# Optimization experiments

Hardware: AMD Instinct MI355X
Metric: run time of the kernel (lower is better)

Reference implementation:

```python
import jax, jax.numpy as jnp
import numpy as np

H = 100      # STATE_SIZE
ATT = 100    # ATTENTION_SIZE
E = 32       # EMBEDDINGS_SIZE
V = 50257    # char vocab
TV = 60      # tag vocab
N = 2048     # source length (incl EOS padding)
T = 2048     # target length (incl EOS padding)
TT = 64      # number of tags


def lstm_cell(x, h, c, Wih, Whh, b):
    # torch gate order: i, f, g, o
    z = x @ Wih.T + h @ Whh.T + b
    i, f, g, o = jnp.split(z, 4)
    c = jax.nn.sigmoid(f) * c + jax.nn.sigmoid(i) * jnp.tanh(g)
    h = jax.nn.sigmoid(o) * jnp.tanh(c)
    return h, c


def lstm_scan(xs, Wih, Whh, b):
    Hs = Whh.shape[1]
    def step(carry, x):
        h, c = lstm_cell(x, carry[0], carry[1], Wih, Whh, b)
        return (h, c), h
    init = (jnp.zeros(Hs, xs.dtype), jnp.zeros(Hs, xs.dtype))
    _, ys = jax.lax.scan(step, init, xs)
    return ys


def setup_inputs() -> dict:
    key = jax.random.key(0)
    ks = iter(jax.random.split(key, 40))
    def rn(shape, s=0.1):
        return jax.random.normal(next(ks), shape, jnp.float32) * s
    return {
        "src_ids": jax.random.randint(next(ks), (1, N), 0, V),
        "tag_ids": jax.random.randint(next(ks), (1, TT), 0, TV),
        "out_ids": jax.random.randint(next(ks), (1, T), 0, V),
        "weight": jnp.ones((), jnp.float32),
        "emb_char": rn((V, E)),
        "emb_tag": rn((TV, E)),
        "enc_f_Wih": rn((4 * H, E)), "enc_f_Whh": rn((4 * H, H)), "enc_f_b": rn((4 * H,)),
        "enc_b_Wih": rn((4 * H, E)), "enc_b_Whh": rn((4 * H, H)), "enc_b_b": rn((4 * H,)),
        "tag_Wih": rn((4 * H, E)), "tag_Whh": rn((4 * H, H)), "tag_b": rn((4 * H,)),
        "dec_Wih": rn((4 * H, 3 * H + E)), "dec_Whh": rn((4 * H, H)), "dec_b": rn((4 * H,)),
        "attn_w1": rn((ATT, 2 * H)), "attn_w2": rn((ATT, 2 * H)), "attn_w3": rn((ATT, 5)),
        "attn_v": rn((1, ATT)),
        "tag_attn_w1": rn((ATT, H)), "tag_attn_w2": rn((ATT, 2 * H)), "tag_attn_v": rn((1, ATT)),
        "out_W": rn((V, H)), "out_b": rn((V,)),
    }


def reference(src_ids, tag_ids, out_ids, weight, emb_char, emb_tag,
              enc_f_Wih, enc_f_Whh, enc_f_b, enc_b_Wih, enc_b_Whh, enc_b_b,
              tag_Wih, tag_Whh, tag_b, dec_Wih, dec_Whh, dec_b,
              attn_w1, attn_w2, attn_w3, attn_v,
              tag_attn_w1, tag_attn_w2, tag_attn_v, out_W, out_b):
    x = emb_char[src_ids[0]]                       # (N, E)
    tg = emb_tag[tag_ids[0]]                       # (TT, E)
    # bidirectional char encoder
    yf = lstm_scan(x, enc_f_Wih, enc_f_Whh, enc_f_b)
    yb = lstm_scan(x[::-1], enc_b_Wih, enc_b_Whh, enc_b_b)[::-1]
    enc = jnp.concatenate([yf, yb], -1)            # (N, 2H)
    # tag encoder + self-attention residual (matches self_encode_tags)
    tv = lstm_scan(tg, tag_Wih, tag_Whh, tag_b)    # (TT, H)
    sa = jax.nn.softmax(tv @ tv.T, axis=-1)
    tagv = tv + jnp.einsum('sh,st->th', tv, sa)    # (TT, H)
    w1dt = enc @ attn_w1.T                         # (N, ATT)
    tag_w1dt = tagv @ tag_attn_w1.T                # (TT, ATT)
    eos_emb = emb_char[0]
    # initial decoder step on (enc_last, tag_last, eos_emb) with zero state
    x0 = jnp.concatenate([enc[-1], tagv[-1], eos_emb])
    h0, c0 = lstm_cell(x0, jnp.zeros(H, jnp.float32), jnp.zeros(H, jnp.float32),
                       dec_Wih, dec_Whh, dec_b)
    # teacher forcing: previous output embedding (EOS=id 0 at t=0)
    prev_ids = jnp.concatenate([jnp.zeros((1,), out_ids.dtype), out_ids[0, :-1]])
    prev_emb = emb_char[prev_ids]                  # (T, E)

    def step(carry, inp):
        h, c, prev_att = carry
        pe, oid = inp
        state = jnp.concatenate([h, c])            # (2H,)
        # tag attention
        taw = jax.nn.softmax(jnp.tanh(tag_w1dt + state @ tag_attn_w2.T) @ tag_attn_v[0])
        tag_ctx = taw @ tagv                       # (H,)
        new_state = state + jnp.concatenate([tag_ctx, tag_ctx])
        # char attention with 5-wide previous-attention feature
        scores = jnp.tanh(w1dt + new_state @ attn_w2.T + prev_att @ attn_w3.T) @ attn_v[0]
        aw = jax.nn.softmax(scores)                # (N,)
        ctx = aw @ enc                             # (2H,)
        startt = jnp.clip(jnp.argmax(aw) - 1, 0, N - 6)
        new_prev = jax.lax.dynamic_slice(aw, (startt,), (5,))
        hn, cn = lstm_cell(jnp.concatenate([ctx, tag_ctx, pe]), h, c,
                           dec_Wih, dec_Whh, dec_b)
        logits = hn @ out_W.T + out_b              # (V,)
        lt = -jax.nn.log_softmax(logits)[oid]
        return (hn, cn, new_prev), lt

    _, losses = jax.lax.scan(step, (h0, c0, jnp.zeros(5, jnp.float32)),
                             (prev_emb, out_ids[0]))
    return jnp.sum(losses) * weight
```

## Files before the change

### kernel.cpp

```cpp
#include <hip/hip_runtime.h>
#include <math.h>

#define NN   2048
#define TLEN 2048
#define TTAG 64
#define VOC  50257
#define GW   32
#define CHK  64
#define RECU 80
static_assert(GW * CHK == NN, "chunking");

#define OFF_XF    0
#define OFF_XB    (OFF_XF  + NN*400)
#define OFF_TGX   (OFF_XB  + NN*400)
#define OFF_PEW   (OFF_TGX + TTAG*400)
#define OFF_ENC   (OFF_PEW + TLEN*400)
#define OFF_W1DT  (OFF_ENC + NN*200)
#define OFF_TAGV  (OFF_W1DT+ NN*100)
#define OFF_TGW1  (OFF_TAGV+ TTAG*100)
#define OFF_TGW   (OFF_TGW1+ TTAG*100)
#define OFF_HOUT  (OFF_TGW + TTAG*400)
#define OFF_REC   (OFF_HOUT+ TLEN*100)
#define OFF_HC    (OFF_REC + 2*GW*RECU*2)
#define OFF_FLG   (OFF_HC  + 2*128*2)
#define OFF_PB    (OFF_FLG + 4096)


__device__ __forceinline__ float rcpf(float x){ return __builtin_amdgcn_rcpf(x); }
__device__ __forceinline__ float sigf(float x){ return rcpf(1.0f+__expf(-x)); }
__device__ __forceinline__ float tanhfast(float x){
  float e = __expf(2.0f*x);
  return 1.0f - 2.0f*rcpf(e+1.0f);
}
__device__ __forceinline__ unsigned short f2b(float x){
  unsigned b=__float_as_uint(x);
  return (unsigned short)((b + 0x7fffu + ((b>>16)&1u))>>16);
}
__device__ __forceinline__ unsigned pk2(float a,float b){ return (unsigned)f2b(a) | ((unsigned)f2b(b)<<16); }
__device__ __forceinline__ float blo(unsigned u){ return __uint_as_float(u<<16); }
__device__ __forceinline__ float bhi(unsigned u){ return __uint_as_float(u&0xffff0000u); }

__device__ __forceinline__ unsigned long long ald64(const unsigned long long* p){
  return __hip_atomic_load(p,__ATOMIC_RELAXED,__HIP_MEMORY_SCOPE_SYSTEM);
}
__device__ __forceinline__ void ast64(unsigned long long* p, unsigned long long v){
  __hip_atomic_store(p,v,__ATOMIC_RELAXED,__HIP_MEMORY_SCOPE_SYSTEM);
}
__device__ __forceinline__ void vm0(){ asm volatile("s_waitcnt vmcnt(0)" ::: "memory"); }

__global__ void kInit(float* ws){
  unsigned long long* f = (unsigned long long*)(ws + OFF_FLG);
  int i = blockIdx.x*256 + threadIdx.x;
  if (i < 2048) ast64(f+i, 0ull);
}

__global__ __launch_bounds__(512) void kPrep(
    const int* src, const int* tag, const int* oid,
    const float* emb_char, const float* emb_tag,
    const float* fWih, const float* fb,
    const float* bWih, const float* bb,
    const float* tWih, const float* tb,
    const float* dWih, const float* db, float* ws)
{
  int r = blockIdx.x, j = threadIdx.x;
  if (j >= 400) return;
  if (r < NN) {
    const float* e = emb_char + (size_t)src[r]*32;
    const float* Wr = fWih + j*32;
    float a = fb[j];
    #pragma unroll
    for (int q=0;q<32;q++) a += e[q]*Wr[q];
    ws[OFF_XF + r*400 + j] = a;
  } else if (r < 2*NN) {
    int n = r - NN;
    const float* e = emb_char + (size_t)src[n]*32;
    const float* Wr = bWih + j*32;
    float a = bb[j];
    #pragma unroll
    for (int q=0;q<32;q++) a += e[q]*Wr[q];
    ws[OFF_XB + n*400 + j] = a;
  } else if (r < 2*NN + TTAG) {
    int s = r - 2*NN;
    const float* e = emb_tag + (size_t)tag[s]*32;
    const float* Wr = tWih + j*32;
    float a = tb[j];
    #pragma unroll
    for (int q=0;q<32;q++) a += e[q]*Wr[q];
    ws[OFF_TGX + s*400 + j] = a;
  } else {
    int t = r - (2*NN + TTAG);
    int pid = (t==0) ? 0 : oid[t-1];
    const float* e = emb_char + (size_t)pid*32;
    const float* Wr = dWih + (size_t)j*332 + 300;
    float a = db[j];
    #pragma unroll
    for (int q=0;q<32;q++) a += e[q]*Wr[q];
    ws[OFF_PEW + t*400 + j] = a;
  }
}

struct EncShared {
  float tvs[TTAG*100];
  float sa [TTAG*64];
  float hbuf[100];
  float zbuf[400];
};

__device__ void lstm_block(const float* Whh, const float* xbase, float* ws,
                           int reverse, int col, EncShared* sh)
{
  int tid = threadIdx.x;
  float whh[100];
  if (tid < 400){
    #pragma unroll
    for (int k=0;k<100;k++) whh[k] = Whh[tid*100+k];
  }
  float c = 0.f;
  if (tid < 100) sh->hbuf[tid] = 0.f;
  __syncthreads();
  for (int i=0;i<NN;i++){
    int n = reverse ? (NN-1-i) : i;
    if (tid < 400){
      float z = xbase[n*400+tid];
      #pragma unroll
      for (int k=0;k<100;k++) z += whh[k]*sh->hbuf[k];
      sh->zbuf[tid] = z;
    }
    __syncthreads();
    if (tid < 100){
      float zi=sh->zbuf[tid], zf=sh->zbuf[tid+100], zg=sh->zbuf[tid+200], zo=sh->zbuf[tid+300];
      c = sigf(zf)*c + sigf(zi)*tanhfast(zg);
      float h = sigf(zo)*tanhfast(c);
      sh->hbuf[tid] = h;
      ws[OFF_ENC + n*200 + col + tid] = h;
    }
    __syncthreads();
  }
}

__global__ __launch_bounds__(512,1) void kEnc(
    const float* fWhh, const float* bWhh, const float* tWhh,
    const float* taw1, const float* dWih, float* ws)
{
  __shared__ EncShared sh;
  int b = blockIdx.x, tid = threadIdx.x;
  if (b == 0){ lstm_block(fWhh, ws+OFF_XF, ws, 0, 0,   &sh); return; }
  if (b == 1){ lstm_block(bWhh, ws+OFF_XB, ws, 1, 100, &sh); return; }

  {
    float whh[100];
    if (tid<400){
      #pragma unroll
      for (int k=0;k<100;k++) whh[k] = tWhh[tid*100+k];
    }
    float c = 0.f;
    if (tid<100) sh.hbuf[tid] = 0.f;
    __syncthreads();
    for (int s=0;s<TTAG;s++){
      if (tid<400){
        float z = ws[OFF_TGX + s*400 + tid];
        #pragma unroll
        for (int k=0;k<100;k++) z += whh[k]*sh.hbuf[k];
        sh.zbuf[tid] = z;
      }
      __syncthreads();
      if (tid<100){
        float zi=sh.zbuf[tid], zf=sh.zbuf[tid+100], zg=sh.zbuf[tid+200], zo=sh.zbuf[tid+300];
        c = sigf(zf)*c + sigf(zi)*tanhfast(zg);
        float h = sigf(zo)*tanhfast(c);
        sh.hbuf[tid] = h;
        sh.tvs[s*100+tid] = h;
      }
      __syncthreads();
    }
  }
  for (int idx=tid; idx<TTAG*TTAG; idx+=512){
    int s=idx>>6, t2=idx&63;
    float a=0.f;
    #pragma unroll 10
    for (int h=0;h<100;h++) a += sh.tvs[s*100+h]*sh.tvs[t2*100+h];
    sh.sa[idx]=a;
  }
  __syncthreads();
  if (tid<TTAG){
    float m=-1e30f;
    for (int t2=0;t2<64;t2++) m = fmaxf(m, sh.sa[tid*64+t2]);
    float sum=0.f;
    for (int t2=0;t2<64;t2++){ float e=__expf(sh.sa[tid*64+t2]-m); sh.sa[tid*64+t2]=e; sum+=e; }
    float r=1.f/sum;
    for (int t2=0;t2<64;t2++) sh.sa[tid*64+t2]*=r;
  }
  __syncthreads();
  float tvloc[13]; int cnt=0;
  for (int idx=tid; idx<TTAG*100; idx+=512){
    int t2=idx/100, hh=idx%100;
    float a = sh.tvs[t2*100+hh];
    for (int s=0;s<64;s++) a += sh.tvs[s*100+hh]*sh.sa[s*64+t2];
    tvloc[cnt++]=a;
    ws[OFF_TAGV+idx]=a;
  }
  __syncthreads();
  float* tagvs = sh.sa;
  cnt=0;
  for (int idx=tid; idx<TTAG*100; idx+=512) tagvs[idx]=tvloc[cnt++];
  __syncthreads();
  for (int idx=tid; idx<TTAG*100; idx+=512){
    int s=idx/100, k=idx%100;
    float a=0.f;
    #pragma unroll 10
    for (int h=0;h<100;h++) a += tagvs[s*100+h]*taw1[k*100+h];
    ws[OFF_TGW1+idx]=a;
  }
  for (int idx=tid; idx<TTAG*400; idx+=512){
    int s=idx/400, j=idx%400;
    const float* Wr = dWih + (size_t)j*332 + 200;
    float a=0.f;
    #pragma unroll 10
    for (int h=0;h<100;h++) a += tagvs[s*100+h]*Wr[h];
    ws[OFF_TGW+idx]=a;
  }
}

__global__ void kMid(const float* aw1, float* ws){
  __shared__ float er[200];
  int n=blockIdx.x, tid=threadIdx.x;
  for (int i=tid;i<200;i+=128) er[i]=ws[OFF_ENC+n*200+i];
  __syncthreads();
  if (tid<100){
    const float* Wr = aw1 + tid*200;
    float a=0.f;
    #pragma unroll 8
    for (int d=0;d<200;d++) a += er[d]*Wr[d];
    ws[OFF_W1DT + n*100 + tid]=a;
  }
}

__global__ __launch_bounds__(512) void kDec(
    const float* dWhh, const float* dWih,
    const float* aw2, const float* aw3, const float* av,
    const float* taw2, const float* tav, float* ws)
{
  __shared__ unsigned aw2L[100*101];
  __shared__ unsigned tw2L[100*101];
  __shared__ unsigned tw1L[TTAG*51];
  __shared__ unsigned tagvL[TTAG*51];
  __shared__ unsigned w1L[CHK*51];
  __shared__ unsigned encL[CHK*101];
  __shared__ float tavL[100], avL[100], aw3L[500];
  __shared__ float hL[100], cL[100], tcL[100], tsaL[100], nsL[200];
  __shared__ float uL[TTAG], tawL[TTAG];
  __shared__ float ctxL[200], a23L[100], ctxpL[200];
  __shared__ float srowL[CHK], eRL[CHK];
  __shared__ float sclL[GW];
  __shared__ float zOwnL[16];
  __shared__ float hdrL[4];
  __shared__ float prevL[5];
  __shared__ float MS[2];
  __shared__ int   amiL;

  const int tid = threadIdx.x;
  const int w   = blockIdx.x;
  unsigned long long* REC = (unsigned long long*)(ws + OFF_REC);
  unsigned long long* HC  = (unsigned long long*)(ws + OFF_HC);
  unsigned long long* FLG = (unsigned long long*)(ws + OFF_FLG);

  const int nu = (w<4)? 4 : 3;
  const int u0 = (w<4)? w*4 : 16 + (w-4)*3;
  const int nact = nu*4;
  const int jslot = tid>>5, l = tid&31;

  unsigned wca0=0,wca1=0,wca2=0,wca3=0, wha0=0,wha1=0, wta0=0,wta1=0;
  int row=0;
  if (jslot < nact){
    row = (jslot&3)*100 + u0 + (jslot>>2);
    const float* Wr = dWih + (size_t)row*332;
    wca0=pk2(Wr[2*l],Wr[2*l+1]);
    wca1=pk2(Wr[2*(32+l)],Wr[2*(32+l)+1]);
    wca2=pk2(Wr[2*(64+l)],Wr[2*(64+l)+1]);
    if (l<4) wca3=pk2(Wr[2*(96+l)],Wr[2*(96+l)+1]);
    const float* Wh = dWhh + (size_t)row*100;
    wha0=pk2(Wh[2*l],Wh[2*l+1]);
    if (l<18) wha1=pk2(Wh[2*(32+l)],Wh[2*(32+l)+1]);
    const float* Wt = Wr + 200;
    wta0=pk2(Wt[2*l],Wt[2*l+1]);
    if (l<18) wta1=pk2(Wt[2*(32+l)],Wt[2*(32+l)+1]);
  }
  for (int i=tid;i<100*100;i+=512){ int k=i/100,p=i%100; aw2L[k*101+p]=pk2(aw2 [k*200+2*p], aw2 [k*200+2*p+1]); }
  for (int i=tid;i<100*100;i+=512){ int k=i/100,p=i%100; tw2L[k*101+p]=pk2(taw2[k*200+2*p], taw2[k*200+2*p+1]); }
  for (int i=tid;i<TTAG*50;i+=512){ int s=i/50,p=i%50; tw1L[s*51+p]=pk2(ws[OFF_TGW1+s*100+2*p], ws[OFF_TGW1+s*100+2*p+1]); }
  for (int i=tid;i<TTAG*50;i+=512){ int s=i/50,p=i%50; tagvL[s*51+p]=pk2(ws[OFF_TAGV+s*100+2*p], ws[OFF_TAGV+s*100+2*p+1]); }
  for (int i=tid;i<CHK*50;i+=512){ int r=i/50,p=i%50; w1L[r*51+p]=pk2(ws[OFF_W1DT+(w*CHK+r)*100+2*p], ws[OFF_W1DT+(w*CHK+r)*100+2*p+1]); }
  for (int i=tid;i<CHK*100;i+=512){ int r=i/100,p=i%100; encL[r*101+p]=pk2(ws[OFF_ENC+(w*CHK+r)*200+2*p], ws[OFF_ENC+(w*CHK+r)*200+2*p+1]); }
  if (tid<100){ tavL[tid]=tav[tid]; avL[tid]=av[tid]; }
  for (int i=tid;i<500;i+=512) aw3L[i]=aw3[i];
  if (tid<5)   prevL[tid]=0.f;
  if (tid<200) ctxL[tid]=ws[OFF_ENC + 2047*200 + tid];
  __syncthreads();

  if (jslot < nact){
    float acc=0.f;
    { unsigned u=wca0; acc += ctxL[2*l]*blo(u) + ctxL[2*l+1]*bhi(u); }
    { unsigned u=wca1; acc += ctxL[2*(32+l)]*blo(u) + ctxL[2*(32+l)+1]*bhi(u); }
    { unsigned u=wca2; acc += ctxL[2*(64+l)]*blo(u) + ctxL[2*(64+l)+1]*bhi(u); }
    if (l<4){ unsigned u=wca3; acc += ctxL[2*(96+l)]*blo(u) + ctxL[2*(96+l)+1]*bhi(u); }
    acc += __shfl_xor(acc,1,32); acc += __shfl_xor(acc,2,32);
    acc += __shfl_xor(acc,4,32); acc += __shfl_xor(acc,8,32); acc += __shfl_xor(acc,16,32);
    if (l==0) zOwnL[jslot] = acc + ws[OFF_TGW + 63*400 + row] + ws[OFF_PEW + row];
  }
  __syncthreads();
  if (tid < 64){
    if (tid < nu){
      float zi=zOwnL[tid*4+0], zg=zOwnL[tid*4+2], zo=zOwnL[tid*4+3];
      float cc = sigf(zi)*tanhfast(zg);
      float hh = sigf(zo)*tanhfast(cc);
      int u = u0+tid;
      ast64(HC + 128 + u, (unsigned long long)__float_as_uint(hh)
                        | ((unsigned long long)__float_as_uint(cc)<<32));
    }
    vm0();
    if (tid==0) ast64(FLG + (size_t)(64 + GW + w)*16, 1ull);
  }

  for (int t=0; t<TLEN; ++t){
    const unsigned sq = (unsigned)(t+1);
    unsigned long long* slot = REC + (size_t)(t&1)*GW*RECU;
    unsigned long long* hcg  = HC + (size_t)((t+1)&1)*128;
    unsigned long long* hcp  = HC + (size_t)(t&1)*128;
    unsigned long long* fr   = FLG + (size_t)(t&1)*GW*16;
    unsigned long long* fhg  = FLG + (size_t)(64 + ((t+1)&1)*GW)*16;

    if (tid < 64){
      int ok = (tid >= GW) ? 1 : 0;
      for(;;){
        if (!ok) ok = ((unsigned)ald64(fhg + (size_t)tid*16) == sq);
        if (__all(ok)) break;
      }
      if (tid < 50){
        unsigned long long v0 = ald64(hcg + 2*tid), v1 = ald64(hcg + 2*tid + 1);
        hL[2*tid]   = __uint_as_float((unsigned)v0); cL[2*tid]   = __uint_as_float((unsigned)(v0>>32));
        hL[2*tid+1] = __uint_as_float((unsigned)v1); cL[2*tid+1] = __uint_as_float((unsigned)(v1>>32));
      }
    }
    __syncthreads();
    if (tid<400){
      int k=tid>>2, q=tid&3, off=q*50;
      const float* sb = (off<100)? (hL+off) : (cL+(off-100));
      float acc=0.f;
      #pragma unroll
      for (int i=0;i<25;i++){ unsigned u=tw2L[k*101+q*25+i]; acc += sb[2*i]*blo(u) + sb[2*i+1]*bhi(u); }
      acc += __shfl_xor(acc,1,4); acc += __shfl_xor(acc,2,4);
      if (q==0) tsaL[k]=acc;
    }
    __syncthreads();
    {
      int sp=tid>>3, l8=tid&7;
      float acc=0.f;
      for (int k=l8;k<100;k+=8){
        unsigned u=tw1L[sp*51+(k>>1)];
        float w1v=(k&1)? bhi(u) : blo(u);
        acc += tanhfast(w1v + tsaL[k]) * tavL[k];
      }
      acc += __shfl_xor(acc,1,8); acc += __shfl_xor(acc,2,8); acc += __shfl_xor(acc,4,8);
      if (l8==0) uL[sp]=acc;
    }
    __syncthreads();
    if (tid<64){
      float v=uL[tid], m=v;
      for (int d=1;d<64;d<<=1) m=fmaxf(m,__shfl_xor(m,d,64));
      float e=__expf(v-m), ssum=e;
      for (int d=1;d<64;d<<=1) ssum+=__shfl_xor(ssum,d,64);
      tawL[tid]=e*rcpf(ssum);
    }
    __syncthreads();
    if (tid<400){
      int hh=tid>>2, q=tid&3;
      float acc=0.f;
      #pragma unroll
      for (int i=0;i<16;i++){
        int s=q*16+i;
        unsigned u=tagvL[s*51+(hh>>1)];
        acc += tawL[s]*((hh&1)? bhi(u):blo(u));
      }
      acc += __shfl_xor(acc,1,4); acc += __shfl_xor(acc,2,4);
      if (q==0){ tcL[hh]=acc; nsL[hh]=hL[hh]+acc; nsL[100+hh]=cL[hh]+acc; }
    }
    __syncthreads();
    if (tid<400){
      int k=tid>>2, q=tid&3, off=q*50;
      float acc=0.f;
      #pragma unroll
      for (int i=0;i<25;i++){ unsigned u=aw2L[k*101+q*25+i]; acc += nsL[off+2*i]*blo(u) + nsL[off+2*i+1]*bhi(u); }
      acc += __shfl_xor(acc,1,4); acc += __shfl_xor(acc,2,4);
      if (q==0){
        float a3=0.f;
        #pragma unroll
        for (int i=0;i<5;i++) a3 += prevL[i]*aw3L[k*5+i];
        a23L[k]=acc+a3;
      }
    }
    __syncthreads();
    {
      int r=tid>>3, l8=tid&7;
      float acc=0.f;
      for (int k=l8;k<100;k+=8){
        unsigned u=w1L[r*51+(k>>1)];
        float w1v=(k&1)? bhi(u) : blo(u);
        acc += tanhfast(w1v + a23L[k]) * avL[k];
      }
      acc += __shfl_xor(acc,1,8); acc += __shfl_xor(acc,2,8); acc += __shfl_xor(acc,4,8);
      if (l8==0) srowL[r]=acc;
    }
    __syncthreads();
    if (tid<64){
      float v=srowL[tid], m=v;
      for (int d=1;d<64;d<<=1) m=fmaxf(m,__shfl_xor(m,d,64));
      float e=__expf(v-m); eRL[tid]=e;
      float Ss=e;
      for (int d=1;d<64;d<<=1) Ss+=__shfl_xor(Ss,d,64);
      float bv=v; int bi=w*CHK+tid;
      for (int d=1;d<64;d<<=1){
        float ov=__shfl_xor(bv,d,64); int oi=__shfl_xor(bi,d,64);
        if (ov>bv || (ov==bv && oi<bi)){ bv=ov; bi=oi; }
      }
      if (tid==0){ hdrL[0]=m; hdrL[1]=Ss; hdrL[2]=bv; ((int*)hdrL)[3]=bi; }
    }
    __syncthreads();
    if (tid<400){
      int d=tid>>1, hf=tid&1;
      float acc=0.f;
      #pragma unroll 8
      for (int i=0;i<32;i++){
        int rr=hf*32+i;
        unsigned u=encL[rr*101+(d>>1)];
        acc += eRL[rr]*((d&1)? bhi(u):blo(u));
      }
      acc += __shfl_xor(acc,1,2);
      if (hf==0) ctxpL[d]=acc;
    }
    __syncthreads();

    #define ZPRE_ROW() do{ \
      if (jslot < nact){ \
        float acc=0.f; \
        { unsigned u=wha0; acc += hL[2*l]*blo(u) + hL[2*l+1]*bhi(u); } \
        if (l<18){ unsigned u=wha1; acc += hL[2*(32+l)]*blo(u) + hL[2*(32+l)+1]*bhi(u); } \
        { unsigned u=wta0; acc += tcL[2*l]*blo(u) + tcL[2*l+1]*bhi(u); } \
        if (l<18){ unsigned u=wta1; acc += tcL[2*(32+l)]*blo(u) + tcL[2*(32+l)+1]*bhi(u); } \
        acc += __shfl_xor(acc,1,32); acc += __shfl_xor(acc,2,32); \
        acc += __shfl_xor(acc,4,32); acc += __shfl_xor(acc,8,32); acc += __shfl_xor(acc,16,32); \
        if (l==0) zOwnL[jslot] = acc + ws[OFF_PEW + t*400 + row]; \
      } \
    }while(0)

    if (tid < 448){
      ZPRE_ROW();
    } else {
      int lane = tid-448;
      unsigned long long* rp = slot + (size_t)w*RECU;
      if (lane < 50)
        ast64(rp+lane, (unsigned long long)pk2(ctxpL[4*lane],ctxpL[4*lane+1])
                     | ((unsigned long long)pk2(ctxpL[4*lane+2],ctxpL[4*lane+3])<<32));
      else { int j=lane-50;
        ast64(rp+lane, (unsigned long long)pk2(srowL[4*j],srowL[4*j+1])
                     | ((unsigned long long)pk2(srowL[4*j+2],srowL[4*j+3])<<32)); }
      if (lane < 2){ int j=14+lane;
        ast64(rp+64+lane, (unsigned long long)pk2(srowL[4*j],srowL[4*j+1])
                        | ((unsigned long long)pk2(srowL[4*j+2],srowL[4*j+3])<<32)); }
      else if (lane==2)
        ast64(rp+66, (unsigned long long)__float_as_uint(hdrL[0])
                   | ((unsigned long long)__float_as_uint(hdrL[1])<<32));
      else if (lane==3)
        ast64(rp+67, (unsigned long long)__float_as_uint(hdrL[2])
                   | ((unsigned long long)(unsigned)((int*)hdrL)[3]<<32));
      vm0();
      if (lane==0) ast64(fr + (size_t)w*16, (unsigned long long)sq);
      ZPRE_ROW();
    }

    if (tid < 64){
      int ok = (tid >= GW) ? 1 : 0;
      for(;;){
        if (!ok) ok = ((unsigned)ald64(fr + (size_t)tid*16) == sq);
        if (__all(ok)) break;
      }
    }
    __syncthreads();
    unsigned long long pay[4];
    if (tid<400){
      int dw=tid>>3, s8=tid&7;
      #pragma unroll
      for (int i=0;i<4;i++) pay[i]=ald64(slot + (size_t)(s8*4+i)*RECU + dw);
    } else if (tid>=448){
      int lane=tid-448, r=lane&31, up=lane>>5;
      unsigned long long v = ald64(slot + (size_t)r*RECU + 66 + up);
      float x0 = __uint_as_float((unsigned)v);
      float x1 = __uint_as_float((unsigned)(v>>32));
      int   xi = (int)(unsigned)(v>>32);
      float pv = x0; int pi = xi;
      #pragma unroll
      for (int d=1;d<32;d<<=1){
        float ov=__shfl_xor(pv,d,32); int oi=__shfl_xor(pi,d,32);
        if (up){ if (ov>pv || (ov==pv && oi<pi)){ pv=ov; pi=oi; } }
        else   { pv = fmaxf(pv,ov); }
      }
      if (!up){
        float sc = __expf(x0 - pv);
        sclL[r] = sc;
        float ss = sc * x1;
        #pragma unroll
        for (int d=1;d<32;d<<=1) ss += __shfl_xor(ss,d,32);
        if (r==0){ MS[0]=pv; MS[1]=ss; }
      } else {
        if (r==0) amiL = pi;
      }
    }
    __syncthreads();
    if (tid<400){
      float rS = rcpf(MS[1]);
      int dw=tid>>3, s8=tid&7;
      float c0=0.f,c1=0.f,c2=0.f,c3=0.f;
      #pragma unroll
      for (int i=0;i<4;i++){
        float sc=sclL[s8*4+i];
        unsigned lo=(unsigned)pay[i], hi=(unsigned)(pay[i]>>32);
        c0 += blo(lo)*sc; c1 += bhi(lo)*sc;
        c2 += blo(hi)*sc; c3 += bhi(hi)*sc;
      }
      #pragma unroll
      for (int d=1;d<8;d<<=1){
        c0 += __shfl_xor(c0,d,8); c1 += __shfl_xor(c1,d,8);
        c2 += __shfl_xor(c2,d,8); c3 += __shfl_xor(c3,d,8);
      }
      if (s8==0){
        ctxL[4*dw+0]=c0*rS; ctxL[4*dw+1]=c1*rS;
        ctxL[4*dw+2]=c2*rS; ctxL[4*dw+3]=c3*rS;
      }
    }
    __syncthreads();
    if (jslot < nact){
      float acc=0.f;
      { unsigned u=wca0; acc += ctxL[2*l]*blo(u) + ctxL[2*l+1]*bhi(u); }
      { unsigned u=wca1; acc += ctxL[2*(32+l)]*blo(u) + ctxL[2*(32+l)+1]*bhi(u); }
      { unsigned u=wca2; acc += ctxL[2*(64+l)]*blo(u) + ctxL[2*(64+l)+1]*bhi(u); }
      if (l<4){ unsigned u=wca3; acc += ctxL[2*(96+l)]*blo(u) + ctxL[2*(96+l)+1]*bhi(u); }
      acc += __shfl_xor(acc,1,32); acc += __shfl_xor(acc,2,32);
      acc += __shfl_xor(acc,4,32); acc += __shfl_xor(acc,8,32); acc += __shfl_xor(acc,16,32);
      if (l==0) zOwnL[jslot] += acc;
    }
    __syncthreads();
    if (tid>=440 && tid<445){
      int i=tid-440;
      int st = amiL-1; st = st<0?0:st; st = st>NN-6?NN-6:st;
      int g = st+i, r=g>>6, lr=g&63;
      unsigned long long v = ald64(slot + (size_t)r*RECU + 50 + (lr>>2));
      unsigned half = (lr&2)? (unsigned)(v>>32) : (unsigned)v;
      float sc = (lr&1)? bhi(half) : blo(half);
      prevL[i] = __expf(sc - MS[0]) * rcpf(MS[1]);
    }
    if (tid < 64){
      if (tid < nu){
        float zi=zOwnL[tid*4+0], zf=zOwnL[tid*4+1], zg=zOwnL[tid*4+2], zo=zOwnL[tid*4+3];
        int u=u0+tid;
        float cc = sigf(zf)*cL[u] + sigf(zi)*tanhfast(zg);
        float hh = sigf(zo)*tanhfast(cc);
        ast64(hcp+u, (unsigned long long)__float_as_uint(hh)
                   | ((unsigned long long)__float_as_uint(cc)<<32));
        ws[OFF_HOUT + t*100 + u] = hh;
      }
      vm0();
      if (tid==0) ast64(FLG + (size_t)(64 + (t&1)*GW + w)*16, (unsigned long long)(sq+1));
    }
  }
}

__global__ __launch_bounds__(256) void kLoss(const float* outW, const float* outb,
                                             const int* oid, float* ws)
{
  const int b=blockIdx.x, tid=threadIdx.x;
  const int tile=b>>1, hf=b&1, t0=tile*16;
  __shared__ float s_hn[16*100];
  __shared__ int   s_oid[16];
  __shared__ float red[4][16][3];
  for (int i=tid;i<1600;i+=256) s_hn[i]=ws[OFF_HOUT + t0*100 + i];
  if (tid<16) s_oid[tid]=oid[t0+tid];
  __syncthreads();
  const int VSPLIT = 25129;
  int vbeg = hf? VSPLIT : 0;
  int vend = hf? VOC : VSPLIT;
  float rm[16], rs[16], ol[16];
  #pragma unroll
  for (int tt=0;tt<16;tt++){ rm[tt]=-1e30f; rs[tt]=0.f; ol[tt]=-1e30f; }
  for (int v=vbeg+tid; v<vend; v+=256){
    const float4* wr = (const float4*)(outW + (size_t)v*100);
    float acc[16];
    #pragma unroll
    for (int tt=0;tt<16;tt++) acc[tt]=0.f;
    #pragma unroll 5
    for (int q=0;q<25;q++){
      float4 wv = wr[q];
      #pragma unroll
      for (int tt=0;tt<16;tt++){
        float4 hv = *(const float4*)(s_hn + tt*100 + q*4);
        acc[tt] += wv.x*hv.x + wv.y*hv.y + wv.z*hv.z + wv.w*hv.w;
      }
    }
    float bb = outb[v];
    #pragma unroll
    for (int tt=0;tt<16;tt++){
      float lg = acc[tt] + bb;
      if (v == s_oid[tt]) ol[tt] = fmaxf(ol[tt], lg);
      if (lg <= rm[tt]) rs[tt] += __expf(lg - rm[tt]);
      else { rs[tt] = rs[tt]*__expf(rm[tt]-lg) + 1.0f; rm[tt]=lg; }
    }
  }
  int wv2=tid>>6, ln=tid&63;
  #pragma unroll
  for (int tt=0;tt<16;tt++){
    float m=rm[tt], sv=rs[tt], o=ol[tt];
    for (int d=1;d<64;d<<=1){
      float om=__shfl_xor(m,d,64), os=__shfl_xor(sv,d,64), oo=__shfl_xor(o,d,64);
      float M2=fmaxf(m,om);
      sv = sv*__expf(m-M2) + os*__expf(om-M2);
      m=M2; o=fmaxf(o,oo);
    }
    if (ln==0){ red[wv2][tt][0]=m; red[wv2][tt][1]=sv; red[wv2][tt][2]=o; }
  }
  __syncthreads();
  if (tid<16){
    float M=-1e30f;
    for (int q=0;q<4;q++) M=fmaxf(M,red[q][tid][0]);
    float S=0.f, O=-1e30f;
    for (int q=0;q<4;q++){ S += red[q][tid][1]*__expf(red[q][tid][0]-M); O=fmaxf(O,red[q][tid][2]); }
    float* pb = ws + OFF_PB + (((tile*2)+hf)*16 + tid)*4;
    pb[0]=M; pb[1]=S; pb[2]=O;
  }
}

__global__ void kFinal(const float* weight, float* ws, float* out){
  __shared__ float red[256];
  int tid=threadIdx.x;
  float acc=0.f;
  for (int t=tid;t<TLEN;t+=256){
    int tile=t>>4, tt=t&15;
    const float* p0 = ws + OFF_PB + ((tile*2+0)*16+tt)*4;
    const float* p1 = ws + OFF_PB + ((tile*2+1)*16+tt)*4;
    float M=fmaxf(p0[0],p1[0]);
    float S=p0[1]*__expf(p0[0]-M) + p1[1]*__expf(p1[0]-M);
    float O=fmaxf(p0[2],p1[2]);
    acc += (M + logf(S)) - O;
  }
  red[tid]=acc; __syncthreads();
  for (int d=128; d>0; d>>=1){
    if (tid<d) red[tid]+=red[tid+d];
    __syncthreads();
  }
  if (tid==0) out[0]=red[0]*weight[0];
}

extern "C" void kernel_launch(void* const* d_in, const int* in_sizes, int n_in,
                              void* d_out, int out_size, void* d_ws, size_t ws_size,
                              hipStream_t stream) {
  const int*   src      = (const int*)  d_in[0];
  const int*   tag      = (const int*)  d_in[1];
  const int*   oid      = (const int*)  d_in[2];
  const float* weight   = (const float*)d_in[3];
  const float* emb_char = (const float*)d_in[4];
  const float* emb_tag  = (const float*)d_in[5];
  const float* fWih=(const float*)d_in[6],  *fWhh=(const float*)d_in[7],  *fb=(const float*)d_in[8];
  const float* bWih=(const float*)d_in[9],  *bWhh=(const float*)d_in[10], *bb=(const float*)d_in[11];
  const float* tWih=(const float*)d_in[12], *tWhh=(const float*)d_in[13], *tb=(const float*)d_in[14];
  const float* dWih=(const float*)d_in[15], *dWhh=(const float*)d_in[16], *db=(const float*)d_in[17];
  const float* aw1 =(const float*)d_in[18], *aw2=(const float*)d_in[19];
  const float* aw3 =(const float*)d_in[20], *av =(const float*)d_in[21];
  const float* taw1=(const float*)d_in[22], *taw2=(const float*)d_in[23], *tavv=(const float*)d_in[24];
  const float* outW=(const float*)d_in[25], *outb=(const float*)d_in[26];
  float* ws  = (float*)d_ws;
  float* out = (float*)d_out;

  kInit<<<8, 256, 0, stream>>>(ws);
  kPrep<<<2*NN+TTAG+TLEN, 512, 0, stream>>>(src,tag,oid,emb_char,emb_tag,
                                            fWih,fb,bWih,bb,tWih,tb,dWih,db,ws);
  kEnc<<<3,512,0,stream>>>(fWhh,bWhh,tWhh,taw1,dWih,ws);
  kMid<<<NN,128,0,stream>>>(aw1,ws);
  kDec<<<GW,512,0,stream>>>(dWhh,dWih,aw2,aw3,av,taw2,tavv,ws);
  kLoss<<<256,256,0,stream>>>(outW,outb,oid,ws);
  kFinal<<<1,256,0,stream>>>(weight,ws,out);
}
```

Before: 26.08 ms.

## Double decoder block width and fold h/c handoff flags into sequence-tagged payloads

The persistent decoder kernel goes from 512 to 1024 threads per block, and each per-step reduction stage is split across twice as many lanes. The separate per-block flag store plus flag poll for publishing h/c is removed. h and c are now packed as bf16 into the low word and the step sequence number goes into the high word, so consumers spin directly on the payload with s_sleep. The own cell state is kept in a register. This targets per-step serial latency and one global round trip per step, at the cost of bf16 precision for the exchanged c/h and more barrier participants per step.

```diff
diff --git a/kernel.cpp b/kernel.cpp
--- a/kernel.cpp
+++ b/kernel.cpp
@@ -235,7 +235,7 @@
   }
 }
 
-__global__ __launch_bounds__(512) void kDec(
+__global__ __launch_bounds__(1024,1) void kDec(
     const float* dWhh, const float* dWih,
     const float* aw2, const float* aw3, const float* av,
     const float* taw2, const float* tav, float* ws)
@@ -285,14 +285,14 @@
     wta0=pk2(Wt[2*l],Wt[2*l+1]);
     if (l<18) wta1=pk2(Wt[2*(32+l)],Wt[2*(32+l)+1]);
   }
-  for (int i=tid;i<100*100;i+=512){ int k=i/100,p=i%100; aw2L[k*101+p]=pk2(aw2 [k*200+2*p], aw2 [k*200+2*p+1]); }
-  for (int i=tid;i<100*100;i+=512){ int k=i/100,p=i%100; tw2L[k*101+p]=pk2(taw2[k*200+2*p], taw2[k*200+2*p+1]); }
-  for (int i=tid;i<TTAG*50;i+=512){ int s=i/50,p=i%50; tw1L[s*51+p]=pk2(ws[OFF_TGW1+s*100+2*p], ws[OFF_TGW1+s*100+2*p+1]); }
-  for (int i=tid;i<TTAG*50;i+=512){ int s=i/50,p=i%50; tagvL[s*51+p]=pk2(ws[OFF_TAGV+s*100+2*p], ws[OFF_TAGV+s*100+2*p+1]); }
-  for (int i=tid;i<CHK*50;i+=512){ int r=i/50,p=i%50; w1L[r*51+p]=pk2(ws[OFF_W1DT+(w*CHK+r)*100+2*p], ws[OFF_W1DT+(w*CHK+r)*100+2*p+1]); }
-  for (int i=tid;i<CHK*100;i+=512){ int r=i/100,p=i%100; encL[r*101+p]=pk2(ws[OFF_ENC+(w*CHK+r)*200+2*p], ws[OFF_ENC+(w*CHK+r)*200+2*p+1]); }
+  for (int i=tid;i<100*100;i+=1024){ int k=i/100,p=i%100; aw2L[k*101+p]=pk2(aw2 [k*200+2*p], aw2 [k*200+2*p+1]); }
+  for (int i=tid;i<100*100;i+=1024){ int k=i/100,p=i%100; tw2L[k*101+p]=pk2(taw2[k*200+2*p], taw2[k*200+2*p+1]); }
+  for (int i=tid;i<TTAG*50;i+=1024){ int s=i/50,p=i%50; tw1L[s*51+p]=pk2(ws[OFF_TGW1+s*100+2*p], ws[OFF_TGW1+s*100+2*p+1]); }
+  for (int i=tid;i<TTAG*50;i+=1024){ int s=i/50,p=i%50; tagvL[s*51+p]=pk2(ws[OFF_TAGV+s*100+2*p], ws[OFF_TAGV+s*100+2*p+1]); }
+  for (int i=tid;i<CHK*50;i+=1024){ int r=i/50,p=i%50; w1L[r*51+p]=pk2(ws[OFF_W1DT+(w*CHK+r)*100+2*p], ws[OFF_W1DT+(w*CHK+r)*100+2*p+1]); }
+  for (int i=tid;i<CHK*100;i+=1024){ int r=i/100,p=i%100; encL[r*101+p]=pk2(ws[OFF_ENC+(w*CHK+r)*200+2*p], ws[OFF_ENC+(w*CHK+r)*200+2*p+1]); }
   if (tid<100){ tavL[tid]=tav[tid]; avL[tid]=av[tid]; }
-  for (int i=tid;i<500;i+=512) aw3L[i]=aw3[i];
+  for (int i=tid;i<500;i+=1024) aw3L[i]=aw3[i];
   if (tid<5)   prevL[tid]=0.f;
   if (tid<200) ctxL[tid]=ws[OFF_ENC + 2047*200 + tid];
   __syncthreads();
@@ -308,17 +308,13 @@
     if (l==0) zOwnL[jslot] = acc + ws[OFF_TGW + 63*400 + row] + ws[OFF_PEW + row];
   }
   __syncthreads();
-  if (tid < 64){
-    if (tid < nu){
-      float zi=zOwnL[tid*4+0], zg=zOwnL[tid*4+2], zo=zOwnL[tid*4+3];
-      float cc = sigf(zi)*tanhfast(zg);
-      float hh = sigf(zo)*tanhfast(cc);
-      int u = u0+tid;
-      ast64(HC + 128 + u, (unsigned long long)__float_as_uint(hh)
-                        | ((unsigned long long)__float_as_uint(cc)<<32));
-    }
-    vm0();
-    if (tid==0) ast64(FLG + (size_t)(64 + GW + w)*16, 1ull);
+  float cOwn = 0.f;
+  if (tid < nu){
+    float zi=zOwnL[tid*4+0], zg=zOwnL[tid*4+2], zo=zOwnL[tid*4+3];
+    float cc = sigf(zi)*tanhfast(zg);
+    float hh = sigf(zo)*tanhfast(cc);
+    cOwn = cc;
+    ast64(HC + 128 + (u0+tid), (unsigned long long)pk2(hh,cc) | (1ull<<32));
   }
 
   for (int t=0; t<TLEN; ++t){
@@ -327,41 +323,48 @@
     unsigned long long* hcg  = HC + (size_t)((t+1)&1)*128;
     unsigned long long* hcp  = HC + (size_t)(t&1)*128;
     unsigned long long* fr   = FLG + (size_t)(t&1)*GW*16;
-    unsigned long long* fhg  = FLG + (size_t)(64 + ((t+1)&1)*GW)*16;
-
-    if (tid < 64){
-      int ok = (tid >= GW) ? 1 : 0;
-      for(;;){
-        if (!ok) ok = ((unsigned)ald64(fhg + (size_t)tid*16) == sq);
-        if (__all(ok)) break;
-      }
-      if (tid < 50){
-        unsigned long long v0 = ald64(hcg + 2*tid), v1 = ald64(hcg + 2*tid + 1);
-        hL[2*tid]   = __uint_as_float((unsigned)v0); cL[2*tid]   = __uint_as_float((unsigned)(v0>>32));
-        hL[2*tid+1] = __uint_as_float((unsigned)v1); cL[2*tid+1] = __uint_as_float((unsigned)(v1>>32));
-      }
-    }
-    __syncthreads();
-    if (tid<400){
-      int k=tid>>2, q=tid&3, off=q*50;
-      const float* sb = (off<100)? (hL+off) : (cL+(off-100));
+
+    if (tid < 50){
+      const unsigned long long* p0 = hcg + 2*tid;
+      unsigned long long v0, v1;
+      for(;;){ v0=ald64(p0);   if((unsigned)(v0>>32)==sq) break; __builtin_amdgcn_s_sleep(1); }
+      for(;;){ v1=ald64(p0+1); if((unsigned)(v1>>32)==sq) break; __builtin_amdgcn_s_sleep(1); }
+      unsigned lo0=(unsigned)v0, lo1=(unsigned)v1;
+      hL[2*tid]  =blo(lo0); cL[2*tid]  =bhi(lo0);
+      hL[2*tid+1]=blo(lo1); cL[2*tid+1]=bhi(lo1);
+    }
+    __syncthreads();
+    if (tid<800){
+      int k=tid>>3, q=tid&7;
       float acc=0.f;
       #pragma unroll
-      for (int i=0;i<25;i++){ unsigned u=tw2L[k*101+q*25+i]; acc += sb[2*i]*blo(u) + sb[2*i+1]*bhi(u); }
-      acc += __shfl_xor(acc,1,4); acc += __shfl_xor(acc,2,4);
+      for (int i=0;i<13;i++){
+        int p=q*13+i;
+        if (p<100){
+          unsigned u=tw2L[k*101+p];
+          const float* bp = (p<50)? &hL[2*p] : &cL[2*p-100];
+          acc += bp[0]*blo(u) + bp[1]*bhi(u);
+        }
+      }
+      acc += __shfl_xor(acc,1,8); acc += __shfl_xor(acc,2,8); acc += __shfl_xor(acc,4,8);
       if (q==0) tsaL[k]=acc;
     }
     __syncthreads();
     {
-      int sp=tid>>3, l8=tid&7;
+      int sp=tid>>4, l16=tid&15;
       float acc=0.f;
-      for (int k=l8;k<100;k+=8){
-        unsigned u=tw1L[sp*51+(k>>1)];
-        float w1v=(k&1)? bhi(u) : blo(u);
-        acc += tanhfast(w1v + tsaL[k]) * tavL[k];
-      }
-      acc += __shfl_xor(acc,1,8); acc += __shfl_xor(acc,2,8); acc += __shfl_xor(acc,4,8);
-      if (l8==0) uL[sp]=acc;
+      #pragma unroll
+      for (int i=0;i<7;i++){
+        int k=l16+16*i;
+        if (k<100){
+          unsigned u=tw1L[sp*51+(k>>1)];
+          float w1v=(k&1)? bhi(u) : blo(u);
+          acc += tanhfast(w1v + tsaL[k]) * tavL[k];
+        }
+      }
+      acc += __shfl_xor(acc,1,16); acc += __shfl_xor(acc,2,16);
+      acc += __shfl_xor(acc,4,16); acc += __shfl_xor(acc,8,16);
+      if (l16==0) uL[sp]=acc;
     }
     __syncthreads();
     if (tid<64){
@@ -372,25 +375,31 @@
       tawL[tid]=e*rcpf(ssum);
     }
     __syncthreads();
-    if (tid<400){
-      int hh=tid>>2, q=tid&3;
+    if (tid<800){
+      int hh=tid>>3, q=tid&7;
       float acc=0.f;
       #pragma unroll
-      for (int i=0;i<16;i++){
-        int s=q*16+i;
+      for (int i=0;i<8;i++){
+        int s=q*8+i;
         unsigned u=tagvL[s*51+(hh>>1)];
         acc += tawL[s]*((hh&1)? bhi(u):blo(u));
       }
-      acc += __shfl_xor(acc,1,4); acc += __shfl_xor(acc,2,4);
+      acc += __shfl_xor(acc,1,8); acc += __shfl_xor(acc,2,8); acc += __shfl_xor(acc,4,8);
       if (q==0){ tcL[hh]=acc; nsL[hh]=hL[hh]+acc; nsL[100+hh]=cL[hh]+acc; }
     }
     __syncthreads();
-    if (tid<400){
-      int k=tid>>2, q=tid&3, off=q*50;
+    if (tid<800){
+      int k=tid>>3, q=tid&7;
       float acc=0.f;
       #pragma unroll
-      for (int i=0;i<25;i++){ unsigned u=aw2L[k*101+q*25+i]; acc += nsL[off+2*i]*blo(u) + nsL[off+2*i+1]*bhi(u); }
-      acc += __shfl_xor(acc,1,4); acc += __shfl_xor(acc,2,4);
+      for (int i=0;i<13;i++){
+        int p=q*13+i;
+        if (p<100){
+          unsigned u=aw2L[k*101+p];
+          acc += nsL[2*p]*blo(u) + nsL[2*p+1]*bhi(u);
+        }
+      }
+      acc += __shfl_xor(acc,1,8); acc += __shfl_xor(acc,2,8); acc += __shfl_xor(acc,4,8);
       if (q==0){
         float a3=0.f;
         #pragma unroll
@@ -400,15 +409,20 @@
     }
     __syncthreads();
     {
-      int r=tid>>3, l8=tid&7;
+      int r=tid>>4, l16=tid&15;
       float acc=0.f;
-      for (int k=l8;k<100;k+=8){
-        unsigned u=w1L[r*51+(k>>1)];
-        float w1v=(k&1)? bhi(u) : blo(u);
-        acc += tanhfast(w1v + a23L[k]) * avL[k];
-      }
-      acc += __shfl_xor(acc,1,8); acc += __shfl_xor(acc,2,8); acc += __shfl_xor(acc,4,8);
-      if (l8==0) srowL[r]=acc;
+      #pragma unroll
+      for (int i=0;i<7;i++){
+        int k=l16+16*i;
+        if (k<100){
+          unsigned u=w1L[r*51+(k>>1)];
+          float w1v=(k&1)? bhi(u) : blo(u);
+          acc += tanhfast(w1v + a23L[k]) * avL[k];
+        }
+      }
+      acc += __shfl_xor(acc,1,16); acc += __shfl_xor(acc,2,16);
+      acc += __shfl_xor(acc,4,16); acc += __shfl_xor(acc,8,16);
+      if (l16==0) srowL[r]=acc;
     }
     __syncthreads();
     if (tid<64){
@@ -425,37 +439,33 @@
       if (tid==0){ hdrL[0]=m; hdrL[1]=Ss; hdrL[2]=bv; ((int*)hdrL)[3]=bi; }
     }
     __syncthreads();
-    if (tid<400){
-      int d=tid>>1, hf=tid&1;
+    if (tid<800){
+      int d=tid>>2, q=tid&3;
       float acc=0.f;
-      #pragma unroll 8
-      for (int i=0;i<32;i++){
-        int rr=hf*32+i;
+      #pragma unroll
+      for (int i=0;i<16;i++){
+        int rr=q*16+i;
         unsigned u=encL[rr*101+(d>>1)];
         acc += eRL[rr]*((d&1)? bhi(u):blo(u));
       }
-      acc += __shfl_xor(acc,1,2);
-      if (hf==0) ctxpL[d]=acc;
-    }
-    __syncthreads();
-
-    #define ZPRE_ROW() do{ \
-      if (jslot < nact){ \
-        float acc=0.f; \
-        { unsigned u=wha0; acc += hL[2*l]*blo(u) + hL[2*l+1]*bhi(u); } \
-        if (l<18){ unsigned u=wha1; acc += hL[2*(32+l)]*blo(u) + hL[2*(32+l)+1]*bhi(u); } \
-        { unsigned u=wta0; acc += tcL[2*l]*blo(u) + tcL[2*l+1]*bhi(u); } \
-        if (l<18){ unsigned u=wta1; acc += tcL[2*(32+l)]*blo(u) + tcL[2*(32+l)+1]*bhi(u); } \
-        acc += __shfl_xor(acc,1,32); acc += __shfl_xor(acc,2,32); \
-        acc += __shfl_xor(acc,4,32); acc += __shfl_xor(acc,8,32); acc += __shfl_xor(acc,16,32); \
-        if (l==0) zOwnL[jslot] = acc + ws[OFF_PEW + t*400 + row]; \
-      } \
-    }while(0)
-
-    if (tid < 448){
-      ZPRE_ROW();
-    } else {
-      int lane = tid-448;
+      acc += __shfl_xor(acc,1,4); acc += __shfl_xor(acc,2,4);
+      if (q==0) ctxpL[d]=acc;
+    }
+    __syncthreads();
+
+    if (tid < 512){
+      if (jslot < nact){
+        float acc=0.f;
+        { unsigned u=wha0; acc += hL[2*l]*blo(u) + hL[2*l+1]*bhi(u); }
+        if (l<18){ unsigned u=wha1; acc += hL[2*(32+l)]*blo(u) + hL[2*(32+l)+1]*bhi(u); }
+        { unsigned u=wta0; acc += tcL[2*l]*blo(u) + tcL[2*l+1]*bhi(u); }
+        if (l<18){ unsigned u=wta1; acc += tcL[2*(32+l)]*blo(u) + tcL[2*(32+l)+1]*bhi(u); }
+        acc += __shfl_xor(acc,1,32); acc += __shfl_xor(acc,2,32);
+        acc += __shfl_xor(acc,4,32); acc += __shfl_xor(acc,8,32); acc += __shfl_xor(acc,16,32);
+        if (l==0) zOwnL[jslot] = acc + ws[OFF_PEW + t*400 + row];
+      }
+    } else if (tid >= 960){
+      int lane = tid-960;
       unsigned long long* rp = slot + (size_t)w*RECU;
       if (lane < 50)
         ast64(rp+lane, (unsigned long long)pk2(ctxpL[4*lane],ctxpL[4*lane+1])
@@ -474,7 +484,6 @@
                    | ((unsigned long long)(unsigned)((int*)hdrL)[3]<<32));
       vm0();
       if (lane==0) ast64(fr + (size_t)w*16, (unsigned long long)sq);
-      ZPRE_ROW();
     }
 
     if (tid < 64){
@@ -485,13 +494,13 @@
       }
     }
     __syncthreads();
-    unsigned long long pay[4];
-    if (tid<400){
-      int dw=tid>>3, s8=tid&7;
-      #pragma unroll
-      for (int i=0;i<4;i++) pay[i]=ald64(slot + (size_t)(s8*4+i)*RECU + dw);
-    } else if (tid>=448){
-      int lane=tid-448, r=lane&31, up=lane>>5;
+    unsigned long long pay[2];
+    if (tid<800){
+      int dw=tid>>4, s16=tid&15;
+      pay[0]=ald64(slot + (size_t)(s16*2  )*RECU + dw);
+      pay[1]=ald64(slot + (size_t)(s16*2+1)*RECU + dw);
+    } else if (tid>=960){
+      int lane=tid-960, r=lane&31, up=lane>>5;
       unsigned long long v = ald64(slot + (size_t)r*RECU + 66 + up);
       float x0 = __uint_as_float((unsigned)v);
       float x1 = __uint_as_float((unsigned)(v>>32));
@@ -515,23 +524,23 @@
       }
     }
     __syncthreads();
-    if (tid<400){
+    if (tid<800){
       float rS = rcpf(MS[1]);
-      int dw=tid>>3, s8=tid&7;
+      int dw=tid>>4, s16=tid&15;
       float c0=0.f,c1=0.f,c2=0.f,c3=0.f;
       #pragma unroll
-      for (int i=0;i<4;i++){
-        float sc=sclL[s8*4+i];
+      for (int i=0;i<2;i++){
+        float sc=sclL[s16*2+i];
         unsigned lo=(unsigned)pay[i], hi=(unsigned)(pay[i]>>32);
         c0 += blo(lo)*sc; c1 += bhi(lo)*sc;
         c2 += blo(hi)*sc; c3 += bhi(hi)*sc;
       }
       #pragma unroll
-      for (int d=1;d<8;d<<=1){
-        c0 += __shfl_xor(c0,d,8); c1 += __shfl_xor(c1,d,8);
-        c2 += __shfl_xor(c2,d,8); c3 += __shfl_xor(c3,d,8);
-      }
-      if (s8==0){
+      for (int d=1;d<16;d<<=1){
+        c0 += __shfl_xor(c0,d,16); c1 += __shfl_xor(c1,d,16);
+        c2 += __shfl_xor(c2,d,16); c3 += __shfl_xor(c3,d,16);
+      }
+      if (s16==0){
         ctxL[4*dw+0]=c0*rS; ctxL[4*dw+1]=c1*rS;
         ctxL[4*dw+2]=c2*rS; ctxL[4*dw+3]=c3*rS;
       }
@@ -557,18 +566,14 @@
       float sc = (lr&1)? bhi(half) : blo(half);
       prevL[i] = __expf(sc - MS[0]) * rcpf(MS[1]);
     }
-    if (tid < 64){
-      if (tid < nu){
-        float zi=zOwnL[tid*4+0], zf=zOwnL[tid*4+1], zg=zOwnL[tid*4+2], zo=zOwnL[tid*4+3];
-        int u=u0+tid;
-        float cc = sigf(zf)*cL[u] + sigf(zi)*tanhfast(zg);
-        float hh = sigf(zo)*tanhfast(cc);
-        ast64(hcp+u, (unsigned long long)__float_as_uint(hh)
-                   | ((unsigned long long)__float_as_uint(cc)<<32));
-        ws[OFF_HOUT + t*100 + u] = hh;
-      }
-      vm0();
-      if (tid==0) ast64(FLG + (size_t)(64 + (t&1)*GW + w)*16, (unsigned long long)(sq+1));
+    if (tid < nu){
+      float zi=zOwnL[tid*4+0], zf=zOwnL[tid*4+1], zg=zOwnL[tid*4+2], zo=zOwnL[tid*4+3];
+      float cc = sigf(zf)*cOwn + sigf(zi)*tanhfast(zg);
+      float hh = sigf(zo)*tanhfast(cc);
+      cOwn = cc;
+      ast64(hcp + (u0+tid), (unsigned long long)pk2(hh,cc)
+                          | ((unsigned long long)(sq+1)<<32));
+      ws[OFF_HOUT + t*100 + (u0+tid)] = hh;
     }
   }
 }
@@ -682,7 +687,7 @@
                                             fWih,fb,bWih,bb,tWih,tb,dWih,db,ws);
   kEnc<<<3,512,0,stream>>>(fWhh,bWhh,tWhh,taw1,dWih,ws);
   kMid<<<NN,128,0,stream>>>(aw1,ws);
-  kDec<<<GW,512,0,stream>>>(dWhh,dWih,aw2,aw3,av,taw2,tavv,ws);
+  kDec<<<GW,1024,0,stream>>>(dWhh,dWih,aw2,aw3,av,taw2,tavv,ws);
   kLoss<<<256,256,0,stream>>>(outW,outb,oid,ws);
   kFinal<<<1,256,0,stream>>>(weight,ws,out);
 }
```

Result: slower. 30.42 ms (+16.6%).

## Embed sequence tags in h/c slots and split score exchange from context payload

Applied to the files above, without the earlier changes.

Packs h and c as bf16 together with a sequence tag into one 64-bit word, so consumers spin on the data itself rather than on a separate flag plus a data read. The cell state is kept in a register rather than reloaded from shared memory. Score rows and headers are published earlier, under their own flag, before the context payload, and the payload loads move into the reduction loop. This cuts the number of cross-workgroup handshakes and the latency on the serial recurrence, at the cost of bf16 precision for h and c and an extra barrier stage.

```diff
diff --git a/kernel.cpp b/kernel.cpp
--- a/kernel.cpp
+++ b/kernel.cpp
@@ -308,17 +308,13 @@
     if (l==0) zOwnL[jslot] = acc + ws[OFF_TGW + 63*400 + row] + ws[OFF_PEW + row];
   }
   __syncthreads();
-  if (tid < 64){
-    if (tid < nu){
-      float zi=zOwnL[tid*4+0], zg=zOwnL[tid*4+2], zo=zOwnL[tid*4+3];
-      float cc = sigf(zi)*tanhfast(zg);
-      float hh = sigf(zo)*tanhfast(cc);
-      int u = u0+tid;
-      ast64(HC + 128 + u, (unsigned long long)__float_as_uint(hh)
-                        | ((unsigned long long)__float_as_uint(cc)<<32));
-    }
-    vm0();
-    if (tid==0) ast64(FLG + (size_t)(64 + GW + w)*16, 1ull);
+  float cOwn = 0.f;
+  if (tid < nu){
+    float zi=zOwnL[tid*4+0], zg=zOwnL[tid*4+2], zo=zOwnL[tid*4+3];
+    float cc = sigf(zi)*tanhfast(zg);
+    float hh = sigf(zo)*tanhfast(cc);
+    cOwn = cc;
+    ast64(HC + 128 + (u0+tid), (unsigned long long)pk2(hh,cc) | (1ull<<32));
   }
 
   for (int t=0; t<TLEN; ++t){
@@ -327,19 +323,14 @@
     unsigned long long* hcg  = HC + (size_t)((t+1)&1)*128;
     unsigned long long* hcp  = HC + (size_t)(t&1)*128;
     unsigned long long* fr   = FLG + (size_t)(t&1)*GW*16;
-    unsigned long long* fhg  = FLG + (size_t)(64 + ((t+1)&1)*GW)*16;
-
-    if (tid < 64){
-      int ok = (tid >= GW) ? 1 : 0;
-      for(;;){
-        if (!ok) ok = ((unsigned)ald64(fhg + (size_t)tid*16) == sq);
-        if (__all(ok)) break;
-      }
-      if (tid < 50){
-        unsigned long long v0 = ald64(hcg + 2*tid), v1 = ald64(hcg + 2*tid + 1);
-        hL[2*tid]   = __uint_as_float((unsigned)v0); cL[2*tid]   = __uint_as_float((unsigned)(v0>>32));
-        hL[2*tid+1] = __uint_as_float((unsigned)v1); cL[2*tid+1] = __uint_as_float((unsigned)(v1>>32));
-      }
+    unsigned long long* fh   = FLG + (size_t)(64 + (t&1)*GW)*16;
+
+    if (tid < 100){
+      const unsigned long long* p0 = hcg + tid;
+      unsigned long long v;
+      for(;;){ v=ald64(p0); if((unsigned)(v>>32)==sq) break; __builtin_amdgcn_s_sleep(1); }
+      unsigned lo=(unsigned)v;
+      hL[tid]=blo(lo); cL[tid]=bhi(lo);
     }
     __syncthreads();
     if (tid<400){
@@ -436,6 +427,20 @@
       }
       acc += __shfl_xor(acc,1,2);
       if (hf==0) ctxpL[d]=acc;
+    } else if (tid>=448){
+      int lane = tid-448;
+      unsigned long long* rp = slot + (size_t)w*RECU;
+      if (lane < 16){ int j=lane;
+        ast64(rp+50+j, (unsigned long long)pk2(srowL[4*j],srowL[4*j+1])
+                     | ((unsigned long long)pk2(srowL[4*j+2],srowL[4*j+3])<<32));
+      } else if (lane==16)
+        ast64(rp+66, (unsigned long long)__float_as_uint(hdrL[0])
+                   | ((unsigned long long)__float_as_uint(hdrL[1])<<32));
+      else if (lane==17)
+        ast64(rp+67, (unsigned long long)__float_as_uint(hdrL[2])
+                   | ((unsigned long long)(unsigned)((int*)hdrL)[3]<<32));
+      vm0();
+      if (lane==0) ast64(fh + (size_t)w*16, (unsigned long long)sq);
     }
     __syncthreads();
 
@@ -460,36 +465,25 @@
       if (lane < 50)
         ast64(rp+lane, (unsigned long long)pk2(ctxpL[4*lane],ctxpL[4*lane+1])
                      | ((unsigned long long)pk2(ctxpL[4*lane+2],ctxpL[4*lane+3])<<32));
-      else { int j=lane-50;
-        ast64(rp+lane, (unsigned long long)pk2(srowL[4*j],srowL[4*j+1])
-                     | ((unsigned long long)pk2(srowL[4*j+2],srowL[4*j+3])<<32)); }
-      if (lane < 2){ int j=14+lane;
-        ast64(rp+64+lane, (unsigned long long)pk2(srowL[4*j],srowL[4*j+1])
-                        | ((unsigned long long)pk2(srowL[4*j+2],srowL[4*j+3])<<32)); }
-      else if (lane==2)
-        ast64(rp+66, (unsigned long long)__float_as_uint(hdrL[0])
-                   | ((unsigned long long)__float_as_uint(hdrL[1])<<32));
-      else if (lane==3)
-        ast64(rp+67, (unsigned long long)__float_as_uint(hdrL[2])
-                   | ((unsigned long long)(unsigned)((int*)hdrL)[3]<<32));
       vm0();
       if (lane==0) ast64(fr + (size_t)w*16, (unsigned long long)sq);
       ZPRE_ROW();
     }
 
+    if (tid < 64){
+      int ok = (tid >= GW) ? 1 : 0;
+      for(;;){
+        if (!ok) ok = ((unsigned)ald64(fh + (size_t)tid*16) == sq);
+        if (__all(ok)) break;
+      }
+    }
+    __syncthreads();
     if (tid < 64){
       int ok = (tid >= GW) ? 1 : 0;
       for(;;){
         if (!ok) ok = ((unsigned)ald64(fr + (size_t)tid*16) == sq);
         if (__all(ok)) break;
       }
-    }
-    __syncthreads();
-    unsigned long long pay[4];
-    if (tid<400){
-      int dw=tid>>3, s8=tid&7;
-      #pragma unroll
-      for (int i=0;i<4;i++) pay[i]=ald64(slot + (size_t)(s8*4+i)*RECU + dw);
     } else if (tid>=448){
       int lane=tid-448, r=lane&31, up=lane>>5;
       unsigned long long v = ald64(slot + (size_t)r*RECU + 66 + up);
@@ -521,8 +515,9 @@
       float c0=0.f,c1=0.f,c2=0.f,c3=0.f;
       #pragma unroll
       for (int i=0;i<4;i++){
-        float sc=sclL[s8*4+i];
-        unsigned lo=(unsigned)pay[i], hi=(unsigned)(pay[i]>>32);
+        unsigned long long p = ald64(slot + (size_t)(s8*4+i)*RECU + dw);
+        float sc = sclL[s8*4+i];
+        unsigned lo=(unsigned)p, hi=(unsigned)(p>>32);
         c0 += blo(lo)*sc; c1 += bhi(lo)*sc;
         c2 += blo(hi)*sc; c3 += bhi(hi)*sc;
       }
@@ -557,18 +552,14 @@
       float sc = (lr&1)? bhi(half) : blo(half);
       prevL[i] = __expf(sc - MS[0]) * rcpf(MS[1]);
     }
-    if (tid < 64){
-      if (tid < nu){
-        float zi=zOwnL[tid*4+0], zf=zOwnL[tid*4+1], zg=zOwnL[tid*4+2], zo=zOwnL[tid*4+3];
-        int u=u0+tid;
-        float cc = sigf(zf)*cL[u] + sigf(zi)*tanhfast(zg);
-        float hh = sigf(zo)*tanhfast(cc);
-        ast64(hcp+u, (unsigned long long)__float_as_uint(hh)
-                   | ((unsigned long long)__float_as_uint(cc)<<32));
-        ws[OFF_HOUT + t*100 + u] = hh;
-      }
-      vm0();
-      if (tid==0) ast64(FLG + (size_t)(64 + (t&1)*GW + w)*16, (unsigned long long)(sq+1));
+    if (tid < nu){
+      float zi=zOwnL[tid*4+0], zf=zOwnL[tid*4+1], zg=zOwnL[tid*4+2], zo=zOwnL[tid*4+3];
+      float cc = sigf(zf)*cOwn + sigf(zi)*tanhfast(zg);
+      float hh = sigf(zo)*tanhfast(cc);
+      cOwn = cc;
+      ast64(hcp + (u0+tid), (unsigned long long)pk2(hh,cc)
+                          | ((unsigned long long)(sq+1)<<32));
+      ws[OFF_HOUT + t*100 + (u0+tid)] = hh;
     }
   }
 }
```

After: 25.91 ms. No clear change (-0.6%).
